# Optimization experiments

Measured on AMD Instinct MI355X. Metric: run time of the kernel, lower is better.

## Reference

```python
import jax, jax.numpy as jnp
import numpy as np

B, C, H, W = 16, 512, 64, 64
WS = 16            # window size -> N = 256 tokens per window
NH = 16            # num heads, head_dim = 32
HD = C // NH
HID = int((4 * C * 0.5) / 64) * 64   # SwiGLU hidden = 1024
CPB = 512
EPS = 1e-5


def _rel_tables(ws):
    r = np.arange(-(ws - 1), ws, dtype=np.float32)
    tab = np.stack(np.meshgrid(r, r, indexing='ij'), axis=-1)  # (2ws-1,2ws-1,2)
    tab = tab / (ws - 1)
    tab = tab * 8.0
    tab = np.sign(tab) * np.log2(np.abs(tab) + 1.0) / np.log2(8.0)
    # relative position index (N,N)
    coords = np.stack(np.meshgrid(np.arange(ws), np.arange(ws), indexing='ij'))
    cf = coords.reshape(2, -1)
    rel = (cf[:, :, None] - cf[:, None, :]).transpose(1, 2, 0).astype(np.int64)
    rel[:, :, 0] += ws - 1
    rel[:, :, 1] += ws - 1
    rel[:, :, 0] *= 2 * ws - 1
    idx = rel.sum(-1)
    return tab.reshape(-1, 2), idx


def setup_inputs() -> dict:
    key = jax.random.key(0)
    ks = jax.random.split(key, 12)
    s = 0.02
    tab, idx = _rel_tables(WS)
    return {
        'x': jax.random.normal(ks[0], (B, C, H, W), jnp.float32),
        'rel_table': jnp.asarray(tab),
        'norm1_w': jnp.ones((C,), jnp.float32),
        'norm1_b': jnp.zeros((C,), jnp.float32),
        'norm2_w': jnp.ones((C,), jnp.float32),
        'norm2_b': jnp.zeros((C,), jnp.float32),
        'qkv_w': jax.random.normal(ks[1], (C, 3 * C), jnp.float32) * s,
        'proj_w': jax.random.normal(ks[2], (C, C), jnp.float32) * s,
        'cpb_w1': jax.random.normal(ks[3], (2, CPB), jnp.float32) * s,
        'cpb_b1': jnp.zeros((CPB,), jnp.float32),
        'cpb_w2': jax.random.normal(ks[4], (CPB, NH), jnp.float32) * s,
        'fc1_w': jax.random.normal(ks[5], (C, 2 * HID), jnp.float32) * s,
        'fc2_w': jax.random.normal(ks[6], (HID, C), jnp.float32) * s,
        'rel_index': jnp.asarray(idx),
    }


def _ln(x, w, b):
    m = jnp.mean(x, axis=-1, keepdims=True)
    v = jnp.mean(jnp.square(x - m), axis=-1, keepdims=True)
    return (x - m) * jax.lax.rsqrt(v + EPS) * w + b


def reference(x, rel_table, norm1_w, norm1_b, norm2_w, norm2_b, qkv_w, proj_w,
              cpb_w1, cpb_b1, cpb_w2, fc1_w, fc2_w, rel_index):
    ws, nh, hd = WS, NH, HD
    N = ws * ws
    # window partition: (B,C,H,W) -> (B*nW, N, C)
    xw = x.reshape(B, C, H // ws, ws, W // ws, ws)
    xw = xw.transpose(0, 2, 4, 3, 5, 1).reshape(-1, N, C)
    Bw = xw.shape[0]

    # --- window attention ---
    h = _ln(xw, norm1_w, norm1_b)
    qkv = (h @ qkv_w).reshape(Bw, N, 3, nh, hd).transpose(2, 0, 3, 1, 4)
    q, k, v = qkv[0], qkv[1], qkv[2]          # (Bw, nh, N, hd)
    attn = jnp.einsum('bhnd,bhmd->bhnm', q, k) * (hd ** -0.5)
    # Swin-v2 continuous position bias MLP + gather
    bias_tab = jax.nn.relu(rel_table @ cpb_w1 + cpb_b1) @ cpb_w2   # ((2ws-1)^2, nh)
    bias = bias_tab[rel_index]                 # (N, N, nh)
    bias = 16.0 * jax.nn.sigmoid(bias.transpose(2, 0, 1))          # (nh, N, N)
    attn = jax.nn.softmax(attn + bias[None], axis=-1)
    o = jnp.einsum('bhnm,bhmd->bhnd', attn, v)
    o = o.transpose(0, 2, 1, 3).reshape(Bw, N, C) @ proj_w
    xw = xw + o

    # --- SwiGLU MLP ---
    h2 = _ln(xw, norm2_w, norm2_b)
    u = h2 @ fc1_w
    val, gate = jnp.split(u, 2, axis=-1)       # Mlp/SwiGLU: chunk -> silu(gate)*x
    xw = xw + (jax.nn.silu(gate) * val) @ fc2_w

    # window reverse + outer skip
    xr = xw.reshape(B, H // ws, W // ws, ws, ws, C)
    xr = xr.transpose(0, 5, 1, 3, 2, 4).reshape(B, C, H, W)
    return xr + x
```

## Files before the change

### kernel.cpp

```cpp
#include <hip/hip_runtime.h>
#include <hip/hip_bf16.h>

typedef unsigned short u16;
typedef unsigned int u32;
typedef __attribute__((ext_vector_type(8))) u16 u16x8;
typedef __attribute__((ext_vector_type(4))) u16 u16x4;
typedef __attribute__((ext_vector_type(8))) short bf16x8;
typedef __attribute__((ext_vector_type(4))) float f32x4;

__device__ __forceinline__ u16 f2bf(float f) {
  u32 u = __float_as_uint(f);
  u += 0x7fffu + ((u >> 16) & 1u);
  return (u16)(u >> 16);
}
__device__ __forceinline__ float bf2f(u16 h) {
  return __uint_as_float(((u32)h) << 16);
}
__device__ __forceinline__ u16 cvt_bf(float f) {
  __hip_bfloat16 h(f);
  return __builtin_bit_cast(u16, h);
}
__device__ __forceinline__ bf16x8 ld_bf8(const u16* p) {
  return __builtin_bit_cast(bf16x8, *(const u16x8*)p);
}

#if __has_builtin(__builtin_amdgcn_exp2f)
#define EXP2(x) __builtin_amdgcn_exp2f(x)
#else
#define EXP2(x) exp2f(x)
#endif

typedef const void __attribute__((address_space(1)))* gas_t;
typedef void __attribute__((address_space(3)))* las_t;
#define GLOAD_LDS16(gp, lp) __builtin_amdgcn_global_load_lds((gas_t)(gp), (las_t)(lp), 16, 0, 0)

#define QSCALE 0.25503486f
#define BIAS_MUL 23.08312065f

__global__ void wtrans_kernel(const float* __restrict__ in, u16* __restrict__ out, int K, int N) {
  int idx = blockIdx.x * 256 + threadIdx.x;
  if (idx >= K * N) return;
  int n = idx / K, k = idx - n * K;
  out[idx] = f2bf(in[(size_t)k * N + n]);
}

__global__ void wtrans_qkv_kernel(const float* __restrict__ in, u16* __restrict__ out) {
  int idx = blockIdx.x * 256 + threadIdx.x;
  int n = idx >> 9, k = idx & 511;
  float s = n < 512 ? QSCALE : 1.f;
  out[idx] = f2bf(in[(size_t)k * 1536 + n] * s);
}

__global__ void wtrans_fc1_kernel(const float* __restrict__ in, u16* __restrict__ out) {
  int idx = blockIdx.x * 256 + threadIdx.x;
  int n = idx >> 9, k = idx & 511;
  int i = ((n >> 5) << 4) | (n & 15);
  int gsel = (n >> 4) & 1;
  out[idx] = f2bf(in[(size_t)k * 2048 + i + gsel * 1024]);
}

__global__ void cpb_kernel(const float* __restrict__ rt, const float* __restrict__ w1,
                           const float* __restrict__ b1, const float* __restrict__ w2,
                           float* __restrict__ tab2) {
  __shared__ float hid[512];
  __shared__ float part[16][17];
  int tix = blockIdx.x;
  int t = threadIdx.x;
  float r0 = rt[tix * 2], r1 = rt[tix * 2 + 1];
  for (int j = t; j < 512; j += 256) {
    float v = r0 * w1[j] + r1 * w1[512 + j] + b1[j];
    hid[j] = v > 0.f ? v : 0.f;
  }
  __syncthreads();
  int hh = t & 15, seg = t >> 4;
  float acc = 0.f;
  for (int j = seg * 32; j < seg * 32 + 32; ++j) acc += hid[j] * w2[j * 16 + hh];
  part[seg][hh] = acc;
  __syncthreads();
  if (t < 16) {
    float s = 0.f;
    for (int g = 0; g < 16; ++g) s += part[g][t];
    tab2[t * 961 + tix] = BIAS_MUL / (1.f + __expf(-s)) - 23.0f;
  }
}

__global__ __launch_bounds__(256, 4) void ln1_kernel(
    const float* __restrict__ x, const float* __restrict__ w, const float* __restrict__ b,
    u16* __restrict__ hbuf) {
  __shared__ u16 tile[512 * 33];
  __shared__ float red[2][8][32];
  __shared__ float meanv[32], rstdv[32];
  int bi = blockIdx.x;
  int bimg = bi >> 7, rest = bi & 127, hrow = rest >> 1, half = rest & 1;
  int t = threadIdx.x, p = t & 31, g = t >> 5;
  const float* xr = x + (size_t)bimg * 512 * 4096 + (size_t)hrow * 64 + half * 32;
  float s = 0.f, s2 = 0.f;
  for (int i = 0; i < 64; ++i) {
    int c = g * 64 + i;
    float v = xr[(size_t)c * 4096 + p];
    tile[c * 33 + p] = f2bf(v);
    s += v; s2 += v * v;
  }
  red[0][g][p] = s; red[1][g][p] = s2;
  __syncthreads();
  if (t < 32) {
    float ss = 0.f, qq = 0.f;
    for (int gg = 0; gg < 8; ++gg) { ss += red[0][gg][t]; qq += red[1][gg][t]; }
    float mu = ss * (1.f / 512.f);
    float var = qq * (1.f / 512.f) - mu * mu;
    meanv[t] = mu;
    rstdv[t] = rsqrtf(var + 1e-5f);
  }
  __syncthreads();
  int c0 = t * 2;
  float w0 = w[c0], w1v = w[c0 + 1], b0 = b[c0], b1v = b[c0 + 1];
  int hy = hrow >> 4, iy = hrow & 15;
  for (int pp = 0; pp < 32; ++pp) {
    int pixel = half * 32 + pp;
    int wx = pixel >> 4, ix = pixel & 15;
    int widx = bimg * 16 + hy * 4 + wx;
    size_t basep = ((size_t)widx * 256 + iy * 16 + ix) * 512;
    u16 rb0 = tile[c0 * 33 + pp], rb1 = tile[(c0 + 1) * 33 + pp];
    float mu = meanv[pp], rs = rstdv[pp];
    float v0 = bf2f(rb0), v1 = bf2f(rb1);
    u16 h0 = f2bf((v0 - mu) * rs * w0 + b0);
    u16 h1 = f2bf((v1 - mu) * rs * w1v + b1v);
    *(u32*)(hbuf + basep + c0) = (u32)h0 | ((u32)h1 << 16);
  }
}

template <int EPI>
__global__ __launch_bounds__(256, 4) void gemm_bt(
    const u16* __restrict__ A, const u16* __restrict__ Bt,
    u16* __restrict__ out, const u16* __restrict__ res,
    const float* __restrict__ xg, float* __restrict__ outf,
    int M, int N, int K) {
  __shared__ u16 As[128 * 64];
  __shared__ u16 Bs[128 * 64];
  const int t = threadIdx.x, l = t & 63, wv = t >> 6;
  const int nbx = N >> 7;
  const int wg = (int)blockIdx.x;
  const int xcd = wg & 7, c = wg >> 3;
  const int cm = c / nbx;
  const int m0 = (xcd * 64 + cm) * 128, n0 = (c - cm * nbx) * 128;
  const int wr = wv >> 1, wc = wv & 1;
  const int lr = l & 15, lk = l >> 4;
  f32x4 acc[4][4] = {};
  for (int kt = 0; kt < K; kt += 64) {
#pragma unroll
    for (int j = 0; j < 4; ++j) {
      int qi = j * 256 + t;
      int r = qi >> 3, c8 = (qi & 7) * 8;
      GLOAD_LDS16(A + (size_t)(m0 + r) * K + kt + c8, As + (size_t)(j * 256 + wv * 64) * 8);
    }
#pragma unroll
    for (int j = 0; j < 4; ++j) {
      int qi = j * 256 + t;
      int r = qi >> 3, c8 = (qi & 7) * 8;
      GLOAD_LDS16(Bt + (size_t)(n0 + r) * K + kt + c8, Bs + (size_t)(j * 256 + wv * 64) * 8);
    }
    __syncthreads();
#pragma unroll
    for (int ks = 0; ks < 2; ++ks) {
      bf16x8 a[4], bb[4];
#pragma unroll
      for (int mf = 0; mf < 4; ++mf)
        a[mf] = ld_bf8(As + (wr * 64 + mf * 16 + lr) * 64 + ks * 32 + lk * 8);
#pragma unroll
      for (int nf = 0; nf < 4; ++nf)
        bb[nf] = ld_bf8(Bs + (wc * 64 + nf * 16 + lr) * 64 + ks * 32 + lk * 8);
#pragma unroll
      for (int mf = 0; mf < 4; ++mf)
#pragma unroll
        for (int nf = 0; nf < 4; ++nf)
          acc[mf][nf] = __builtin_amdgcn_mfma_f32_16x16x32_bf16(a[mf], bb[nf], acc[mf][nf], 0, 0, 0);
    }
    __syncthreads();
  }
#pragma unroll
  for (int mf = 0; mf < 4; ++mf) {
    int rbase = m0 + wr * 64 + mf * 16 + lk * 4;
    if constexpr (EPI == 3) {
#pragma unroll
      for (int nf = 0; nf < 4; nf += 2) {
        int colv = n0 + wc * 64 + nf * 16 + lr;
        int i = ((colv >> 5) << 4) | (colv & 15);
#pragma unroll
        for (int jj = 0; jj < 4; ++jj) {
          int row = rbase + jj;
          float val = acc[mf][nf][jj], gate = acc[mf][nf + 1][jj];
          float sil = gate / (1.f + __expf(-gate));
          out[(size_t)row * 1024 + i] = f2bf(sil * val);
        }
      }
    } else if constexpr (EPI == 4 || EPI == 5) {
      int widx = rbase >> 8, iy = (rbase >> 4) & 15, ix0 = rbase & 15;
      int bimg = widx >> 4, hy = (widx >> 2) & 3, wx = widx & 3;
#pragma unroll
      for (int nf = 0; nf < 4; ++nf) {
        int col = n0 + wc * 64 + nf * 16 + lr;
        size_t obase = (((size_t)(bimg * 512 + col) * 64) + hy * 16 + iy) * 64 + wx * 16 + ix0;
        const float* xp = xg + obase;
        if constexpr (EPI == 4) {
          float* op = outf + obase;
#pragma unroll
          for (int jj = 0; jj < 4; ++jj)
            op[jj] = acc[mf][nf][jj] + bf2f(res[(size_t)(rbase + jj) * 512 + col]) + xp[jj];
        } else {
#pragma unroll
          for (int jj = 0; jj < 4; ++jj)
            out[(size_t)(rbase + jj) * 512 + col] = f2bf(acc[mf][nf][jj] + xp[jj]);
        }
      }
    } else {
#pragma unroll
      for (int nf = 0; nf < 4; ++nf) {
        int col = n0 + wc * 64 + nf * 16 + lr;
#pragma unroll
        for (int jj = 0; jj < 4; ++jj)
          out[(size_t)(rbase + jj) * N + col] = f2bf(acc[mf][nf][jj]);
      }
    }
  }
}

__global__ __launch_bounds__(256, 4) void attn_kernel(
    const u16* __restrict__ qkv, const float* __restrict__ tab2, u16* __restrict__ ob) {
  __shared__ u16 vt[32 * 72];
  __shared__ float tabh4[31 * 32 * 4];
  __shared__ u16 pl[4][16 * 76];
  const int h = blockIdx.x, w = blockIdx.y;
  const int t = threadIdx.x, l = t & 63, wid = t >> 6;
  const u16* qg = qkv + (size_t)(w * 256) * 1536 + h * 32;
  const u16* kg = qg + 512;
  const u16* vg = qg + 1024;
  const float* th = tab2 + h * 961;
  for (int i = t; i < 992; i += 256) {
    int dy = i >> 5, dx = i & 31;
#pragma unroll
    for (int r = 0; r < 4; ++r) {
      int dxr = dx + r;
      tabh4[i * 4 + r] = (dxr <= 30) ? th[dy * 31 + dxr] : 0.f;
    }
  }
  const int q4 = l >> 4, c0 = l & 15;
  const int dx0 = q4 * 4 - c0 + 15;
  bf16x8 qa[4];
#pragma unroll
  for (int mf = 0; mf < 4; ++mf)
    qa[mf] = ld_bf8(qg + (size_t)(wid * 64 + mf * 16 + c0) * 1536 + q4 * 8);
  f32x4 oacc[4][2] = {};
  float psum[4][4] = {};
  for (int ct = 0; ct < 4; ++ct) {
    {
      int r = t & 63, j = t >> 6;
      u16x8 dv = *(const u16x8*)(vg + (size_t)(ct * 64 + r) * 1536 + j * 8);
#pragma unroll
      for (int e = 0; e < 8; ++e) vt[(j * 8 + e) * 72 + r] = dv[e];
    }
    __syncthreads();
    bf16x8 bfr[4];
#pragma unroll
    for (int nf = 0; nf < 4; ++nf)
      bfr[nf] = ld_bf8(kg + (size_t)(ct * 64 + nf * 16 + c0) * 1536 + q4 * 8);
    bf16x8 vfr[2][2];
#pragma unroll
    for (int df = 0; df < 2; ++df)
#pragma unroll
      for (int ks2 = 0; ks2 < 2; ++ks2)
        vfr[df][ks2] = ld_bf8(vt + (df * 16 + c0) * 72 + ks2 * 32 + q4 * 8);
#pragma unroll
    for (int mf = 0; mf < 4; ++mf) {
      const int dyb = wid * 4 + mf - ct * 4 + 15;
      f32x4 sacc[4];
#pragma unroll
      for (int nf = 0; nf < 4; ++nf)
        sacc[nf] = *(const f32x4*)&tabh4[((dyb - nf) * 32 + dx0) * 4];
      __builtin_amdgcn_s_setprio(1);
#pragma unroll
      for (int nf = 0; nf < 4; ++nf)
        sacc[nf] = __builtin_amdgcn_mfma_f32_16x16x32_bf16(qa[mf], bfr[nf], sacc[nf], 0, 0, 0);
      __builtin_amdgcn_s_setprio(0);
#pragma unroll
      for (int nf = 0; nf < 4; ++nf) {
#pragma unroll
        for (int jj = 0; jj < 4; ++jj) {
          float p = EXP2(sacc[nf][jj]);
          psum[mf][jj] += p;
          pl[wid][(q4 * 4 + jj) * 76 + nf * 16 + c0] = cvt_bf(p);
        }
      }
      __builtin_amdgcn_s_setprio(1);
#pragma unroll
      for (int ks2 = 0; ks2 < 2; ++ks2) {
        bf16x8 pa = ld_bf8(&pl[wid][c0 * 76 + ks2 * 32 + q4 * 8]);
        oacc[mf][0] = __builtin_amdgcn_mfma_f32_16x16x32_bf16(pa, vfr[0][ks2], oacc[mf][0], 0, 0, 0);
        oacc[mf][1] = __builtin_amdgcn_mfma_f32_16x16x32_bf16(pa, vfr[1][ks2], oacc[mf][1], 0, 0, 0);
      }
      __builtin_amdgcn_s_setprio(0);
    }
    __syncthreads();
  }
#pragma unroll
  for (int mf = 0; mf < 4; ++mf) {
#pragma unroll
    for (int jj = 0; jj < 4; ++jj) {
      float s = psum[mf][jj];
      s += __shfl_xor(s, 1);
      s += __shfl_xor(s, 2);
      s += __shfl_xor(s, 4);
      s += __shfl_xor(s, 8);
      float inv = 1.f / s;
      int row = wid * 64 + mf * 16 + q4 * 4 + jj;
      size_t obase = ((size_t)w * 256 + row) * 512 + h * 32;
      ob[obase + c0] = f2bf(oacc[mf][0][jj] * inv);
      ob[obase + 16 + c0] = f2bf(oacc[mf][1][jj] * inv);
    }
  }
}

__global__ __launch_bounds__(256, 4) void ln2_kernel(const u16* __restrict__ r1,
    const float* __restrict__ w, const float* __restrict__ b, u16* __restrict__ h2) {
  int t = threadIdx.x, l = t & 63, wid = t >> 6;
  size_t token = (size_t)blockIdx.x * 4 + wid;
  const u16* rp = r1 + token * 512 + l * 8;
  u16x8 raw = *(const u16x8*)rp;
  float v[8]; float s = 0.f, s2 = 0.f;
#pragma unroll
  for (int i = 0; i < 8; ++i) { v[i] = bf2f(raw[i]); s += v[i]; s2 += v[i] * v[i]; }
#pragma unroll
  for (int m = 1; m < 64; m <<= 1) { s += __shfl_xor(s, m); s2 += __shfl_xor(s2, m); }
  float mu = s * (1.f / 512.f);
  float var = s2 * (1.f / 512.f) - mu * mu;
  float rs = rsqrtf(var + 1e-5f);
  u16x8 o;
#pragma unroll
  for (int i = 0; i < 8; ++i) {
    int c = l * 8 + i;
    o[i] = f2bf((v[i] - mu) * rs * w[c] + b[c]);
  }
  *(u16x8*)(h2 + token * 512 + l * 8) = o;
}

extern "C" void kernel_launch(void* const* d_in, const int* in_sizes, int n_in,
                              void* d_out, int out_size, void* d_ws, size_t ws_size,
                              hipStream_t stream) {
  (void)in_sizes; (void)n_in; (void)out_size; (void)ws_size;
  const float* x = (const float*)d_in[0];
  const float* rel_table = (const float*)d_in[1];
  const float* n1w = (const float*)d_in[2];
  const float* n1b = (const float*)d_in[3];
  const float* n2w = (const float*)d_in[4];
  const float* n2b = (const float*)d_in[5];
  const float* qkv_w = (const float*)d_in[6];
  const float* proj_w = (const float*)d_in[7];
  const float* cpb_w1 = (const float*)d_in[8];
  const float* cpb_b1 = (const float*)d_in[9];
  const float* cpb_w2 = (const float*)d_in[10];
  const float* fc1_w = (const float*)d_in[11];
  const float* fc2_w = (const float*)d_in[12];
  float* outp = (float*)d_out;
  char* ws = (char*)d_ws;

  u16* wq = (u16*)(ws + 0);
  u16* wp = (u16*)(ws + 1572864);
  u16* w1 = (u16*)(ws + 2097152);
  u16* w2 = (u16*)(ws + 4194304);
  float* tab2 = (float*)(ws + 5242880);
  const size_t RB = 67108864;
  u16* R1 = (u16*)(ws + 8388608 + RB);
  u16* R2 = (u16*)(ws + 8388608 + 2 * RB);
  u16* R3 = (u16*)(ws + 8388608 + 3 * RB);
  u16* R4 = (u16*)(ws + 8388608 + 4 * RB);

  wtrans_qkv_kernel<<<3072, 256, 0, stream>>>(qkv_w, wq);
  wtrans_kernel<<<1024, 256, 0, stream>>>(proj_w, wp, 512, 512);
  wtrans_fc1_kernel<<<4096, 256, 0, stream>>>(fc1_w, w1);
  wtrans_kernel<<<2048, 256, 0, stream>>>(fc2_w, w2, 1024, 512);
  cpb_kernel<<<961, 256, 0, stream>>>(rel_table, cpb_w1, cpb_b1, cpb_w2, tab2);
  ln1_kernel<<<2048, 256, 0, stream>>>(x, n1w, n1b, R2);
  gemm_bt<0><<<6144, 256, 0, stream>>>(R2, wq, R3, nullptr,
                                       nullptr, nullptr, 65536, 1536, 512);
  attn_kernel<<<dim3(16, 256), 256, 0, stream>>>(R3, tab2, R2);
  gemm_bt<5><<<2048, 256, 0, stream>>>(R2, wp, R1, nullptr,
                                       x, nullptr, 65536, 512, 512);
  ln2_kernel<<<16384, 256, 0, stream>>>(R1, n2w, n2b, R3);
  gemm_bt<3><<<8192, 256, 0, stream>>>(R3, w1, R4, nullptr,
                                       nullptr, nullptr, 65536, 2048, 512);
  gemm_bt<4><<<2048, 256, 0, stream>>>(R4, w2, nullptr, R1,
                                       x, outp, 65536, 512, 1024);
}
```

Baseline: 746.7 us.

## Fuse weight-prep kernels and read window-ordered bf16 residual in proj GEMM

The five weight-transpose and CPB kernels are merged into one launch that branches on block index, cutting launch overhead. ln1 now also writes the bf16 input in window-major order to a new buffer. The proj GEMM epilogue reads that buffer, coalesced row-major, in place of gathering fp32 x with a strided NCHW scatter. The cost is an extra 64 MB bf16 write in ln1 plus a read in the GEMM, and the residual is now rounded to bf16.

```diff
diff --git a/kernel.cpp b/kernel.cpp
--- a/kernel.cpp
+++ b/kernel.cpp
@@ -37,56 +37,59 @@
 #define QSCALE 0.25503486f
 #define BIAS_MUL 23.08312065f
 
-__global__ void wtrans_kernel(const float* __restrict__ in, u16* __restrict__ out, int K, int N) {
-  int idx = blockIdx.x * 256 + threadIdx.x;
-  if (idx >= K * N) return;
-  int n = idx / K, k = idx - n * K;
-  out[idx] = f2bf(in[(size_t)k * N + n]);
-}
-
-__global__ void wtrans_qkv_kernel(const float* __restrict__ in, u16* __restrict__ out) {
-  int idx = blockIdx.x * 256 + threadIdx.x;
-  int n = idx >> 9, k = idx & 511;
-  float s = n < 512 ? QSCALE : 1.f;
-  out[idx] = f2bf(in[(size_t)k * 1536 + n] * s);
-}
-
-__global__ void wtrans_fc1_kernel(const float* __restrict__ in, u16* __restrict__ out) {
-  int idx = blockIdx.x * 256 + threadIdx.x;
-  int n = idx >> 9, k = idx & 511;
-  int i = ((n >> 5) << 4) | (n & 15);
-  int gsel = (n >> 4) & 1;
-  out[idx] = f2bf(in[(size_t)k * 2048 + i + gsel * 1024]);
-}
-
-__global__ void cpb_kernel(const float* __restrict__ rt, const float* __restrict__ w1,
-                           const float* __restrict__ b1, const float* __restrict__ w2,
-                           float* __restrict__ tab2) {
-  __shared__ float hid[512];
-  __shared__ float part[16][17];
-  int tix = blockIdx.x;
-  int t = threadIdx.x;
-  float r0 = rt[tix * 2], r1 = rt[tix * 2 + 1];
-  for (int j = t; j < 512; j += 256) {
-    float v = r0 * w1[j] + r1 * w1[512 + j] + b1[j];
-    hid[j] = v > 0.f ? v : 0.f;
-  }
-  __syncthreads();
-  int hh = t & 15, seg = t >> 4;
-  float acc = 0.f;
-  for (int j = seg * 32; j < seg * 32 + 32; ++j) acc += hid[j] * w2[j * 16 + hh];
-  part[seg][hh] = acc;
-  __syncthreads();
-  if (t < 16) {
-    float s = 0.f;
-    for (int g = 0; g < 16; ++g) s += part[g][t];
-    tab2[t * 961 + tix] = BIAS_MUL / (1.f + __expf(-s)) - 23.0f;
+__global__ void prep_kernel(
+    const float* __restrict__ qkv_w, const float* __restrict__ proj_w,
+    const float* __restrict__ fc1_w, const float* __restrict__ fc2_w,
+    const float* __restrict__ rt, const float* __restrict__ cw1,
+    const float* __restrict__ cb1, const float* __restrict__ cw2,
+    u16* __restrict__ wq, u16* __restrict__ wp, u16* __restrict__ w1,
+    u16* __restrict__ w2, float* __restrict__ tab2) {
+  int b = blockIdx.x, t = threadIdx.x;
+  if (b < 3072) {
+    int idx = b * 256 + t;
+    int n = idx >> 9, k = idx & 511;
+    float s = n < 512 ? QSCALE : 1.f;
+    wq[idx] = f2bf(qkv_w[(size_t)k * 1536 + n] * s);
+  } else if (b < 4096) {
+    int idx = (b - 3072) * 256 + t;
+    int n = idx >> 9, k = idx & 511;
+    wp[idx] = f2bf(proj_w[(size_t)k * 512 + n]);
+  } else if (b < 8192) {
+    int idx = (b - 4096) * 256 + t;
+    int n = idx >> 9, k = idx & 511;
+    int i = ((n >> 5) << 4) | (n & 15);
+    int gsel = (n >> 4) & 1;
+    w1[idx] = f2bf(fc1_w[(size_t)k * 2048 + i + gsel * 1024]);
+  } else if (b < 10240) {
+    int idx = (b - 8192) * 256 + t;
+    int n = idx >> 10, k = idx & 1023;
+    w2[idx] = f2bf(fc2_w[(size_t)k * 512 + n]);
+  } else {
+    __shared__ float hid[512];
+    __shared__ float part[16][17];
+    int tix = b - 10240;
+    float r0 = rt[tix * 2], r1 = rt[tix * 2 + 1];
+    for (int j = t; j < 512; j += 256) {
+      float v = r0 * cw1[j] + r1 * cw1[512 + j] + cb1[j];
+      hid[j] = v > 0.f ? v : 0.f;
+    }
+    __syncthreads();
+    int hh = t & 15, seg = t >> 4;
+    float acc = 0.f;
+    for (int j = seg * 32; j < seg * 32 + 32; ++j) acc += hid[j] * cw2[j * 16 + hh];
+    part[seg][hh] = acc;
+    __syncthreads();
+    if (t < 16) {
+      float s = 0.f;
+      for (int g = 0; g < 16; ++g) s += part[g][t];
+      tab2[t * 961 + tix] = BIAS_MUL / (1.f + __expf(-s)) - 23.0f;
+    }
   }
 }
 
 __global__ __launch_bounds__(256, 4) void ln1_kernel(
     const float* __restrict__ x, const float* __restrict__ w, const float* __restrict__ b,
-    u16* __restrict__ hbuf) {
+    u16* __restrict__ hbuf, u16* __restrict__ xwbuf) {
   __shared__ u16 tile[512 * 33];
   __shared__ float red[2][8][32];
   __shared__ float meanv[32], rstdv[32];
@@ -123,6 +126,7 @@
     u16 rb0 = tile[c0 * 33 + pp], rb1 = tile[(c0 + 1) * 33 + pp];
     float mu = meanv[pp], rs = rstdv[pp];
     float v0 = bf2f(rb0), v1 = bf2f(rb1);
+    *(u32*)(xwbuf + basep + c0) = (u32)rb0 | ((u32)rb1 << 16);
     u16 h0 = f2bf((v0 - mu) * rs * w0 + b0);
     u16 h1 = f2bf((v1 - mu) * rs * w1v + b1v);
     *(u32*)(hbuf + basep + c0) = (u32)h0 | ((u32)h1 << 16);
@@ -193,7 +197,7 @@
           out[(size_t)row * 1024 + i] = f2bf(sil * val);
         }
       }
-    } else if constexpr (EPI == 4 || EPI == 5) {
+    } else if constexpr (EPI == 4) {
       int widx = rbase >> 8, iy = (rbase >> 4) & 15, ix0 = rbase & 15;
       int bimg = widx >> 4, hy = (widx >> 2) & 3, wx = widx & 3;
 #pragma unroll
@@ -201,15 +205,19 @@
         int col = n0 + wc * 64 + nf * 16 + lr;
         size_t obase = (((size_t)(bimg * 512 + col) * 64) + hy * 16 + iy) * 64 + wx * 16 + ix0;
         const float* xp = xg + obase;
-        if constexpr (EPI == 4) {
-          float* op = outf + obase;
-#pragma unroll
-          for (int jj = 0; jj < 4; ++jj)
-            op[jj] = acc[mf][nf][jj] + bf2f(res[(size_t)(rbase + jj) * 512 + col]) + xp[jj];
-        } else {
-#pragma unroll
-          for (int jj = 0; jj < 4; ++jj)
-            out[(size_t)(rbase + jj) * 512 + col] = f2bf(acc[mf][nf][jj] + xp[jj]);
+        float* op = outf + obase;
+#pragma unroll
+        for (int jj = 0; jj < 4; ++jj)
+          op[jj] = acc[mf][nf][jj] + bf2f(res[(size_t)(rbase + jj) * 512 + col]) + xp[jj];
+      }
+    } else if constexpr (EPI == 1) {
+#pragma unroll
+      for (int nf = 0; nf < 4; ++nf) {
+        int col = n0 + wc * 64 + nf * 16 + lr;
+#pragma unroll
+        for (int jj = 0; jj < 4; ++jj) {
+          int row = rbase + jj;
+          out[(size_t)row * N + col] = f2bf(acc[mf][nf][jj] + bf2f(res[(size_t)row * N + col]));
         }
       }
     } else {
@@ -368,22 +376,21 @@
   u16* w2 = (u16*)(ws + 4194304);
   float* tab2 = (float*)(ws + 5242880);
   const size_t RB = 67108864;
+  u16* R0 = (u16*)(ws + 8388608);
   u16* R1 = (u16*)(ws + 8388608 + RB);
   u16* R2 = (u16*)(ws + 8388608 + 2 * RB);
   u16* R3 = (u16*)(ws + 8388608 + 3 * RB);
   u16* R4 = (u16*)(ws + 8388608 + 4 * RB);
 
-  wtrans_qkv_kernel<<<3072, 256, 0, stream>>>(qkv_w, wq);
-  wtrans_kernel<<<1024, 256, 0, stream>>>(proj_w, wp, 512, 512);
-  wtrans_fc1_kernel<<<4096, 256, 0, stream>>>(fc1_w, w1);
-  wtrans_kernel<<<2048, 256, 0, stream>>>(fc2_w, w2, 1024, 512);
-  cpb_kernel<<<961, 256, 0, stream>>>(rel_table, cpb_w1, cpb_b1, cpb_w2, tab2);
-  ln1_kernel<<<2048, 256, 0, stream>>>(x, n1w, n1b, R2);
+  prep_kernel<<<11201, 256, 0, stream>>>(qkv_w, proj_w, fc1_w, fc2_w,
+                                         rel_table, cpb_w1, cpb_b1, cpb_w2,
+                                         wq, wp, w1, w2, tab2);
+  ln1_kernel<<<2048, 256, 0, stream>>>(x, n1w, n1b, R2, R0);
   gemm_bt<0><<<6144, 256, 0, stream>>>(R2, wq, R3, nullptr,
                                        nullptr, nullptr, 65536, 1536, 512);
   attn_kernel<<<dim3(16, 256), 256, 0, stream>>>(R3, tab2, R2);
-  gemm_bt<5><<<2048, 256, 0, stream>>>(R2, wp, R1, nullptr,
-                                       x, nullptr, 65536, 512, 512);
+  gemm_bt<1><<<2048, 256, 0, stream>>>(R2, wp, R1, R0,
+                                       nullptr, nullptr, 65536, 512, 512);
   ln2_kernel<<<16384, 256, 0, stream>>>(R1, n2w, n2b, R3);
   gemm_bt<3><<<8192, 256, 0, stream>>>(R3, w1, R4, nullptr,
                                        nullptr, nullptr, 65536, 2048, 512);
```

New measurement: 746.9 us. About the same (+0.0%).
